# Kernel optimization log

Measured on AMD Instinct MI355X. Metric: run time of the kernel, lower is better.

The kernel has to match this reference:

```python
import jax, jax.numpy as jnp
import numpy as np

N_HEADS = 4
M = 16            # n_points (neighbors kept per voxel)
DIST = 4          # manhattan distance threshold
D_MODEL = 128
D_FFN = 256
D_CHL = 64
GRID = 96         # spatial_shape per axis
LN_EPS = 1e-5
BN_EPS = 1e-3


def setup_inputs() -> dict:
    key = jax.random.key(0)
    ks = jax.random.split(key, 24)
    N = 8192
    w = lambda k, s: jax.random.normal(k, s, jnp.float32) * 0.02
    z = lambda d: jnp.zeros((d,), jnp.float32)
    o = lambda d: jnp.ones((d,), jnp.float32)
    return {
        "features": jax.random.normal(ks[0], (N, D_CHL), jnp.float32),
        "coords": jax.random.randint(ks[1], (N, 3), 0, GRID, jnp.int32),
        "pe_w1": w(ks[2], (3, D_MODEL // 2)), "pe_b1": z(D_MODEL // 2),
        "pe_w2": w(ks[3], (D_MODEL // 2, D_MODEL)), "pe_b2": z(D_MODEL),
        "in_w": w(ks[4], (D_CHL, D_MODEL)), "in_b": z(D_MODEL),
        "q_w": w(ks[5], (D_MODEL, D_MODEL)), "q_b": z(D_MODEL),
        "k_w": w(ks[6], (D_MODEL, D_MODEL)), "k_b": z(D_MODEL),
        "v_w": w(ks[7], (D_MODEL, D_MODEL)), "v_b": z(D_MODEL),
        "o_w": w(ks[8], (D_MODEL, D_MODEL)), "o_b": z(D_MODEL),
        "n1_g": o(D_MODEL), "n1_b": z(D_MODEL),
        "l1_w": w(ks[9], (D_MODEL, D_FFN)), "l1_b": z(D_FFN),
        "l2_w": w(ks[10], (D_FFN, D_MODEL)), "l2_b": z(D_MODEL),
        "n3_g": o(D_MODEL), "n3_b": z(D_MODEL),
        "fu_w": w(ks[11], (D_MODEL + D_CHL, D_CHL)), "fu_b": z(D_CHL),
        "bn_g": o(D_CHL), "bn_b": z(D_CHL),
    }


def _layernorm(x, g, b):
    mu = jnp.mean(x, -1, keepdims=True)
    var = jnp.mean(jnp.square(x - mu), -1, keepdims=True)
    return (x - mu) * jax.lax.rsqrt(var + LN_EPS) * g + b


def reference(features, coords, pe_w1, pe_b1, pe_w2, pe_b2, in_w, in_b,
              q_w, q_b, k_w, k_b, v_w, v_b, o_w, o_b, n1_g, n1_b,
              l1_w, l1_b, l2_w, l2_b, n3_g, n3_b, fu_w, fu_b, bn_g, bn_b):
    N = features.shape[0]
    hd = D_MODEL // N_HEADS
    ci = coords.astype(jnp.float32)
    # input projection + dynamic learnable positional encoding
    src = features @ in_w + in_b
    vc = ci / (GRID - 1.0)
    src = src + (jax.nn.relu(vc @ pe_w1 + pe_b1) @ pe_w2 + pe_b2)
    # pairwise manhattan distances; accumulate per coordinate to avoid [N,N,3]
    dist = jnp.zeros((N, N), jnp.float32)
    for d in range(3):
        dist = dist + jnp.abs(ci[:, d, None] - ci[None, :, d])
    dist = jnp.where(dist <= DIST, dist, jnp.inf)
    neg_top, idx = jax.lax.top_k(-dist, M)          # [N, M]
    valid = neg_top != -jnp.inf
    # gather neighbor features; invalid slots are zero (as in torch)
    nb = jnp.where(valid[:, :, None], src[jnp.where(valid, idx, 0)], 0.0)  # [N,M,D]
    # cross-attention: query is neighbor 0 (self). NOTE: faithful raw .view
    # reshape of [N,M,D] -> [N,H,M,hd] (interleaves neighbor/head axes as torch does)
    q = (nb[:, :1] @ q_w + q_b).reshape(N, N_HEADS, 1, hd)
    k = (nb @ k_w + k_b).reshape(N, N_HEADS, M, hd)
    v = (nb @ v_w + v_b).reshape(N, N_HEADS, M, hd)
    scores = jnp.einsum('nhqd,nhkd->nhqk', q, k) / jnp.sqrt(jnp.float32(D_MODEL))
    attn = jax.nn.softmax(scores, axis=-1)
    head_out = jnp.einsum('nhqk,nhkd->nhqd', attn, v).reshape(N, D_MODEL)
    out = head_out @ o_w + o_b
    tgt = _layernorm(src + out, n1_g, n1_b)
    # FFN
    tgt2 = jax.nn.relu(tgt @ l1_w + l1_b) @ l2_w + l2_b
    tgt = _layernorm(tgt + tgt2, n3_g, n3_b)
    # EnhancedFusion: concat -> linear -> batchnorm (train-mode stats) -> relu
    fused = jnp.concatenate([features, tgt], axis=1) @ fu_w + fu_b
    mu = jnp.mean(fused, 0)
    var = jnp.var(fused, 0)
    fused = (fused - mu) * jax.lax.rsqrt(var + BN_EPS) * bn_g + bn_b
    return jax.nn.relu(fused)
```

## Files before the change

### kernel.cpp

```cpp
#include <hip/hip_runtime.h>

#define DEVFN __device__ __forceinline__

DEVFN float relu(float x) { return x < 0.f ? 0.f : x; }

__global__ __launch_bounds__(256, 4) void ka_pre_cst(
    const float* __restrict__ features, const int* __restrict__ coords,
    const float* __restrict__ pe_w1, const float* __restrict__ pe_b1,
    const float* __restrict__ pe_w2, const float* __restrict__ pe_b2,
    const float* __restrict__ in_w, const float* __restrict__ in_b,
    const float* __restrict__ q_w, const float* __restrict__ k_w,
    const float* __restrict__ v_w,
    float* __restrict__ src,
    float* __restrict__ qs, float* __restrict__ ks, float* __restrict__ vs,
    int* __restrict__ nbr, float* __restrict__ bnAcc, int N)
{
    __shared__ float sF[512];
    __shared__ float sH[512];
    __shared__ float S[1024];
    __shared__ int   sC[24];
    __shared__ int cnt[16];
    __shared__ int lst[16 * 64];
    __shared__ int outL[256];

    const int tid = threadIdx.x;
    const int bx = blockIdx.x;
    const int role_nbr = (bx % 3) == 2;

    if (role_nbr) {
        const int nb = bx / 3;
        const int q0 = nb * 16;
        if (nb == 0 && tid < 128) bnAcc[tid] = 0.f;
        if (tid < 16) cnt[tid] = 0;
        outL[tid] = -1;
        __syncthreads();
        int qx[16], qy[16], qz[16];
#pragma unroll
        for (int q = 0; q < 16; ++q) {
            qx[q] = coords[(q0 + q) * 3 + 0];
            qy[q] = coords[(q0 + q) * 3 + 1];
            qz[q] = coords[(q0 + q) * 3 + 2];
        }
        for (int cd = tid; cd < N; cd += 256) {
            int cx = coords[cd * 3 + 0];
            int cy = coords[cd * 3 + 1];
            int cz = coords[cd * 3 + 2];
#pragma unroll
            for (int q = 0; q < 16; ++q) {
                int dx = cx - qx[q]; dx = dx < 0 ? -dx : dx;
                int dy = cy - qy[q]; dy = dy < 0 ? -dy : dy;
                int dz = cz - qz[q]; dz = dz < 0 ? -dz : dz;
                int d = dx + dy + dz;
                if (d <= 4) {
                    int s = atomicAdd(&cnt[q], 1);
                    if (s < 64) lst[q * 64 + s] = (d << 13) | cd;
                }
            }
        }
        __syncthreads();
        {
            const int q = tid >> 4, t = tid & 15;
            int n = cnt[q]; if (n > 64) n = 64;
            for (int e = t; e < n; e += 16) {
                int key = lst[q * 64 + e];
                int rank = 0;
                for (int j = 0; j < n; ++j) rank += (lst[q * 64 + j] < key) ? 1 : 0;
                if (rank < 16) outL[q * 16 + rank] = key & 8191;
            }
        }
        __syncthreads();
        {
            const int q = tid >> 4, t = tid & 15;
            nbr[(q0 + q) * 16 + t] = outL[q * 16 + t];
        }
        return;
    }

    const int sb = (bx / 3) * 2 + (bx % 3);
    const int r0 = sb * 8;
    if (tid < 24) sC[tid] = coords[r0 * 3 + tid];
    for (int i = tid; i < 512; i += 256) sF[i] = features[r0 * 64 + i];
    __syncthreads();
    for (int i = tid; i < 512; i += 256) {
        int r = i >> 6, t = i & 63;
        float v0 = sC[r * 3 + 0] * (1.f / 95.f);
        float v1 = sC[r * 3 + 1] * (1.f / 95.f);
        float v2 = sC[r * 3 + 2] * (1.f / 95.f);
        float h = v0 * pe_w1[t] + v1 * pe_w1[64 + t] + v2 * pe_w1[128 + t] + pe_b1[t];
        sH[i] = relu(h);
    }
    __syncthreads();
    const int c = tid & 127, rh = tid >> 7;
    {
        float acc[4];
        const float base = in_b[c] + pe_b2[c];
#pragma unroll
        for (int r = 0; r < 4; ++r) acc[r] = base;
        for (int j = 0; j < 64; ++j) {
            float w1 = in_w[j * 128 + c];
            float w2 = pe_w2[j * 128 + c];
#pragma unroll
            for (int r = 0; r < 4; ++r) {
                int rr = rh * 4 + r;
                acc[r] += sF[rr * 64 + j] * w1 + sH[rr * 64 + j] * w2;
            }
        }
#pragma unroll
        for (int r = 0; r < 4; ++r) {
            src[(r0 + rh * 4 + r) * 128 + c] = acc[r];
            S[(rh * 4 + r) * 128 + c] = acc[r];
        }
    }
    __syncthreads();
    {
        float aq[4], ak[4], av[4];
#pragma unroll
        for (int r = 0; r < 4; ++r) { aq[r] = 0.f; ak[r] = 0.f; av[r] = 0.f; }
        for (int k4 = 0; k4 < 32; ++k4) {
            float wq0 = q_w[(k4 * 4 + 0) * 128 + c];
            float wq1 = q_w[(k4 * 4 + 1) * 128 + c];
            float wq2 = q_w[(k4 * 4 + 2) * 128 + c];
            float wq3 = q_w[(k4 * 4 + 3) * 128 + c];
            float wk0 = k_w[(k4 * 4 + 0) * 128 + c];
            float wk1 = k_w[(k4 * 4 + 1) * 128 + c];
            float wk2 = k_w[(k4 * 4 + 2) * 128 + c];
            float wk3 = k_w[(k4 * 4 + 3) * 128 + c];
            float wv0 = v_w[(k4 * 4 + 0) * 128 + c];
            float wv1 = v_w[(k4 * 4 + 1) * 128 + c];
            float wv2 = v_w[(k4 * 4 + 2) * 128 + c];
            float wv3 = v_w[(k4 * 4 + 3) * 128 + c];
#pragma unroll
            for (int r = 0; r < 4; ++r) {
                float4 s = *(const float4*)(&S[(rh * 4 + r) * 128 + k4 * 4]);
                aq[r] += s.x * wq0 + s.y * wq1 + s.z * wq2 + s.w * wq3;
                ak[r] += s.x * wk0 + s.y * wk1 + s.z * wk2 + s.w * wk3;
                av[r] += s.x * wv0 + s.y * wv1 + s.z * wv2 + s.w * wv3;
            }
        }
#pragma unroll
        for (int r = 0; r < 4; ++r) {
            qs[(r0 + rh * 4 + r) * 128 + c] = aq[r];
            ks[(r0 + rh * 4 + r) * 128 + c] = ak[r];
            vs[(r0 + rh * 4 + r) * 128 + c] = av[r];
        }
    }
}

DEVFN void ln_rows8(float* Cb, const float* __restrict__ g,
                    const float* __restrict__ b, int tid)
{
    const int r = tid >> 5, l = tid & 31;
    float x[4]; float s = 0.f, s2 = 0.f;
#pragma unroll
    for (int i = 0; i < 4; ++i) {
        x[i] = Cb[r * 128 + l * 4 + i];
        s += x[i]; s2 += x[i] * x[i];
    }
#pragma unroll
    for (int o = 1; o < 32; o <<= 1) { s += __shfl_xor(s, o); s2 += __shfl_xor(s2, o); }
    float mu = s * (1.f / 128.f);
    float var = s2 * (1.f / 128.f) - mu * mu;
    float rstd = rsqrtf(var + 1e-5f);
#pragma unroll
    for (int i = 0; i < 4; ++i) {
        int cc = l * 4 + i;
        Cb[r * 128 + cc] = (x[i] - mu) * rstd * g[cc] + b[cc];
    }
}

__global__ __launch_bounds__(256, 4) void k4_main_cst(
    const float* __restrict__ features, const float* __restrict__ src,
    const float* __restrict__ qs, const float* __restrict__ ks, const float* __restrict__ vs,
    const int* __restrict__ nbr,
    const float* __restrict__ q_b, const float* __restrict__ k_b,
    const float* __restrict__ v_b,
    const float* __restrict__ o_w, const float* __restrict__ o_b,
    const float* __restrict__ n1_g, const float* __restrict__ n1_b,
    const float* __restrict__ l1_w, const float* __restrict__ l1_b,
    const float* __restrict__ l2_w, const float* __restrict__ l2_b,
    const float* __restrict__ n3_g, const float* __restrict__ n3_b,
    const float* __restrict__ fu_w, const float* __restrict__ fu_b,
    float* __restrict__ fused, float* __restrict__ bnSum, float* __restrict__ bnSq)
{
    __shared__ float A[1024];
    __shared__ float Bt[1024];
    __shared__ float C[1024];
    __shared__ float Q[1024];
    __shared__ float H[2048];
    __shared__ float SC[512];
    __shared__ float F[512];
    __shared__ __align__(16) float bK[128], bV[128];
    __shared__ int idxL[128];
    const int tid = threadIdx.x;
    const int r0 = blockIdx.x * 8;

    for (int i = tid; i < 1024; i += 256) A[i] = src[r0 * 128 + i];
    for (int i = tid; i < 512; i += 256) F[i] = features[r0 * 64 + i];
    if (tid < 128) {
        idxL[tid] = nbr[r0 * 16 + tid];
        bK[tid] = k_b[tid]; bV[tid] = v_b[tid];
    }
    __syncthreads();
    {
        int r = tid >> 5, cg = tid & 31;
        int i0 = idxL[r * 16];
        float4 qv = make_float4(0.f, 0.f, 0.f, 0.f);
        if (i0 >= 0) qv = *(const float4*)(qs + i0 * 128 + cg * 4);
        float4 qb = *(const float4*)(q_b + cg * 4);
        qv.x += qb.x; qv.y += qb.y; qv.z += qb.z; qv.w += qb.w;
        *(float4*)(&Q[r * 128 + cg * 4]) = qv;
    }
    __syncthreads();

    const int ar = tid >> 5, ah = (tid >> 3) & 3, ag = tid & 7;
    {
#pragma unroll
        for (int jj = 0; jj < 2; ++jj) {
            int j = ag + jj * 8;
            int j4 = j >> 2, ch = j & 3;
            int id = idxL[ar * 16 + ah * 4 + j4];
            float s = 0.f;
#pragma unroll
            for (int c4 = 0; c4 < 8; ++c4) {
                float4 qv = *(const float4*)(&Q[ar * 128 + ah * 32 + c4 * 4]);
                float4 kb = *(const float4*)(&bK[ch * 32 + c4 * 4]);
                float4 kv = make_float4(0.f, 0.f, 0.f, 0.f);
                if (id >= 0) kv = *(const float4*)(ks + id * 128 + ch * 32 + c4 * 4);
                s += qv.x * (kv.x + kb.x) + qv.y * (kv.y + kb.y)
                   + qv.z * (kv.z + kb.z) + qv.w * (kv.w + kb.w);
            }
            SC[ar * 64 + ah * 16 + j] = s * 0.08838834764831845f;
        }
    }
    __syncthreads();

    {
        float p[16];
        float mx = -3.4e38f;
#pragma unroll
        for (int j = 0; j < 16; ++j) { p[j] = SC[ar * 64 + ah * 16 + j]; mx = fmaxf(mx, p[j]); }
        float sum = 0.f;
#pragma unroll
        for (int j = 0; j < 16; ++j) { p[j] = __expf(p[j] - mx); sum += p[j]; }
        float inv = 1.f / sum;
        float4 acc = make_float4(0.f, 0.f, 0.f, 0.f);
#pragma unroll
        for (int j = 0; j < 16; ++j) {
            int j4 = j >> 2, ch = j & 3;
            int id = idxL[ar * 16 + ah * 4 + j4];
            float4 vb = *(const float4*)(&bV[ch * 32 + ag * 4]);
            float4 vv = make_float4(0.f, 0.f, 0.f, 0.f);
            if (id >= 0) vv = *(const float4*)(vs + id * 128 + ch * 32 + ag * 4);
            float w = p[j] * inv;
            acc.x += w * (vv.x + vb.x); acc.y += w * (vv.y + vb.y);
            acc.z += w * (vv.z + vb.z); acc.w += w * (vv.w + vb.w);
        }
        *(float4*)(&Bt[ar * 128 + ah * 32 + ag * 4]) = acc;
    }
    __syncthreads();

    {
        const int c = tid & 127, kh = tid >> 7;
        float acc[8];
#pragma unroll
        for (int r = 0; r < 8; ++r) acc[r] = 0.f;
        const float* wp = o_w + kh * 64 * 128 + c;
        for (int k4 = 0; k4 < 16; ++k4) {
            float w0 = wp[(k4 * 4 + 0) * 128];
            float w1 = wp[(k4 * 4 + 1) * 128];
            float w2 = wp[(k4 * 4 + 2) * 128];
            float w3 = wp[(k4 * 4 + 3) * 128];
#pragma unroll
            for (int r = 0; r < 8; ++r) {
                float4 t = *(const float4*)(&Bt[r * 128 + kh * 64 + k4 * 4]);
                acc[r] += t.x * w0 + t.y * w1 + t.z * w2 + t.w * w3;
            }
        }
#pragma unroll
        for (int r = 0; r < 8; ++r) H[kh * 1024 + r * 128 + c] = acc[r];
    }
    __syncthreads();
    for (int i = tid; i < 1024; i += 256) {
        int c = i & 127;
        C[i] = A[i] + o_b[c] + H[i] + H[1024 + i];
    }
    __syncthreads();
    ln_rows8(C, n1_g, n1_b, tid);
    __syncthreads();

    {
        const int f = tid;
        float acc[8];
#pragma unroll
        for (int r = 0; r < 8; ++r) acc[r] = 0.f;
        for (int k4 = 0; k4 < 32; ++k4) {
            float w0 = l1_w[(k4 * 4 + 0) * 256 + f];
            float w1 = l1_w[(k4 * 4 + 1) * 256 + f];
            float w2 = l1_w[(k4 * 4 + 2) * 256 + f];
            float w3 = l1_w[(k4 * 4 + 3) * 256 + f];
#pragma unroll
            for (int r = 0; r < 8; ++r) {
                float4 t = *(const float4*)(&C[r * 128 + k4 * 4]);
                acc[r] += t.x * w0 + t.y * w1 + t.z * w2 + t.w * w3;
            }
        }
        const float bb = l1_b[f];
#pragma unroll
        for (int r = 0; r < 8; ++r) H[r * 256 + f] = relu(acc[r] + bb);
    }
    __syncthreads();

    {
        const int c = tid & 127, kh = tid >> 7;
        float acc[8];
#pragma unroll
        for (int r = 0; r < 8; ++r) acc[r] = 0.f;
        const float* wp = l2_w + kh * 128 * 128 + c;
        for (int k4 = 0; k4 < 32; ++k4) {
            float w0 = wp[(k4 * 4 + 0) * 128];
            float w1 = wp[(k4 * 4 + 1) * 128];
            float w2 = wp[(k4 * 4 + 2) * 128];
            float w3 = wp[(k4 * 4 + 3) * 128];
#pragma unroll
            for (int r = 0; r < 8; ++r) {
                float4 t = *(const float4*)(&H[r * 256 + kh * 128 + k4 * 4]);
                acc[r] += t.x * w0 + t.y * w1 + t.z * w2 + t.w * w3;
            }
        }
        float* P = kh ? Bt : A;
#pragma unroll
        for (int r = 0; r < 8; ++r) P[r * 128 + c] = acc[r];
    }
    __syncthreads();
    for (int i = tid; i < 1024; i += 256) {
        int c = i & 127;
        C[i] += l2_b[c] + A[i] + Bt[i];
    }
    __syncthreads();
    ln_rows8(C, n3_g, n3_b, tid);
    __syncthreads();

    {
        const int c = tid & 63, rg = tid >> 6;
        float acc[2];
        const float fb = fu_b[c];
#pragma unroll
        for (int r = 0; r < 2; ++r) acc[r] = fb;
        for (int j4 = 0; j4 < 16; ++j4) {
            float w0 = fu_w[(j4 * 4 + 0) * 64 + c];
            float w1 = fu_w[(j4 * 4 + 1) * 64 + c];
            float w2 = fu_w[(j4 * 4 + 2) * 64 + c];
            float w3 = fu_w[(j4 * 4 + 3) * 64 + c];
#pragma unroll
            for (int r = 0; r < 2; ++r) {
                float4 t = *(const float4*)(&F[(rg * 2 + r) * 64 + j4 * 4]);
                acc[r] += t.x * w0 + t.y * w1 + t.z * w2 + t.w * w3;
            }
        }
        for (int j4 = 0; j4 < 32; ++j4) {
            float w0 = fu_w[(64 + j4 * 4 + 0) * 64 + c];
            float w1 = fu_w[(64 + j4 * 4 + 1) * 64 + c];
            float w2 = fu_w[(64 + j4 * 4 + 2) * 64 + c];
            float w3 = fu_w[(64 + j4 * 4 + 3) * 64 + c];
#pragma unroll
            for (int r = 0; r < 2; ++r) {
                float4 t = *(const float4*)(&C[(rg * 2 + r) * 128 + j4 * 4]);
                acc[r] += t.x * w0 + t.y * w1 + t.z * w2 + t.w * w3;
            }
        }
#pragma unroll
        for (int r = 0; r < 2; ++r) {
            int row = rg * 2 + r;
            float v = acc[r];
            fused[(r0 + row) * 64 + c] = v;
            H[row * 64 + c] = v;
        }
    }
    __syncthreads();
    if (tid < 64) {
        float s = 0.f, s2 = 0.f;
#pragma unroll
        for (int r = 0; r < 8; ++r) { float x = H[r * 64 + tid]; s += x; s2 += x * x; }
        atomicAdd(&bnSum[tid], s);
        atomicAdd(&bnSq[tid], s2);
    }
}

__global__ __launch_bounds__(256) void k5_bn_cst(
    const float* __restrict__ fused, const float* __restrict__ bnSum,
    const float* __restrict__ bnSq,
    const float* __restrict__ g, const float* __restrict__ b,
    float* __restrict__ out, int N)
{
    const int total = N * 64;
    const float invN = 1.f / (float)N;
    for (int i = blockIdx.x * 256 + threadIdx.x; i < total; i += gridDim.x * 256) {
        int c = i & 63;
        float mu = bnSum[c] * invN;
        float var = bnSq[c] * invN - mu * mu;
        float x = fused[i];
        float y = (x - mu) * rsqrtf(var + 1e-3f) * g[c] + b[c];
        out[i] = relu(y);
    }
}

extern "C" void kernel_launch(void* const* d_in, const int* in_sizes, int n_in,
                              void* d_out, int out_size, void* d_ws, size_t ws_size,
                              hipStream_t stream)
{
    const float* features = (const float*)d_in[0];
    const int*   coords   = (const int*)d_in[1];
    const float* pe_w1 = (const float*)d_in[2];
    const float* pe_b1 = (const float*)d_in[3];
    const float* pe_w2 = (const float*)d_in[4];
    const float* pe_b2 = (const float*)d_in[5];
    const float* in_w  = (const float*)d_in[6];
    const float* in_b  = (const float*)d_in[7];
    const float* q_w   = (const float*)d_in[8];
    const float* q_b   = (const float*)d_in[9];
    const float* k_w   = (const float*)d_in[10];
    const float* k_b   = (const float*)d_in[11];
    const float* v_w   = (const float*)d_in[12];
    const float* v_b   = (const float*)d_in[13];
    const float* o_w   = (const float*)d_in[14];
    const float* o_b   = (const float*)d_in[15];
    const float* n1_g  = (const float*)d_in[16];
    const float* n1_b  = (const float*)d_in[17];
    const float* l1_w  = (const float*)d_in[18];
    const float* l1_b  = (const float*)d_in[19];
    const float* l2_w  = (const float*)d_in[20];
    const float* l2_b  = (const float*)d_in[21];
    const float* n3_g  = (const float*)d_in[22];
    const float* n3_b  = (const float*)d_in[23];
    const float* fu_w  = (const float*)d_in[24];
    const float* fu_b  = (const float*)d_in[25];
    const float* bn_g  = (const float*)d_in[26];
    const float* bn_b  = (const float*)d_in[27];

    const int N = in_sizes[0] / 64;

    float* src   = (float*)d_ws;
    float* qs    = src + (size_t)N * 128;
    float* ks    = qs  + (size_t)N * 128;
    float* vs    = ks  + (size_t)N * 128;
    float* fused = vs  + (size_t)N * 128;
    int*   nbr    = (int*)(fused + (size_t)N * 64);
    float* bnSum  = (float*)(nbr + (size_t)N * 16);
    float* bnSq   = bnSum + 64;

    ka_pre_cst<<<N / 8 + N / 16, 256, 0, stream>>>(features, coords,
                                                   pe_w1, pe_b1, pe_w2, pe_b2,
                                                   in_w, in_b, q_w, k_w, v_w,
                                                   src, qs, ks, vs, nbr, bnSum, N);
    k4_main_cst<<<N / 8, 256, 0, stream>>>(features, src, qs, ks, vs, nbr,
                                           q_b, k_b, v_b, o_w, o_b, n1_g, n1_b,
                                           l1_w, l1_b, l2_w, l2_b, n3_g, n3_b,
                                           fu_w, fu_b, fused, bnSum, bnSq);
    k5_bn_cst<<<512, 256, 0, stream>>>(fused, bnSum, bnSq, bn_g, bn_b,
                                       (float*)d_out, N);
}
```

Baseline: 221.3 us.

## Halve rows per block in main kernel to double grid and occupancy

The fused attention/FFN/fusion kernel now handles 4 voxels per block instead of 8, doubling the grid to N/4 blocks and raising the launch-bounds occupancy hint from 4 to 8 blocks. Shared memory buffers are halved and every thread-to-work mapping is reworked: scores, attention-value accumulation (2 channels per thread), layernorm over 64-lane groups, and the matmuls with 4 rows. The aim is more parallelism and better latency hiding for the gather-heavy attention. In exchange each weight read from global or L2 is reused across fewer rows, so total weight traffic doubles, and the vector loads become scalar loads.

```diff
diff --git a/kernel.cpp b/kernel.cpp
--- a/kernel.cpp
+++ b/kernel.cpp
@@ -146,29 +146,7 @@
     }
 }
 
-DEVFN void ln_rows8(float* Cb, const float* __restrict__ g,
-                    const float* __restrict__ b, int tid)
-{
-    const int r = tid >> 5, l = tid & 31;
-    float x[4]; float s = 0.f, s2 = 0.f;
-#pragma unroll
-    for (int i = 0; i < 4; ++i) {
-        x[i] = Cb[r * 128 + l * 4 + i];
-        s += x[i]; s2 += x[i] * x[i];
-    }
-#pragma unroll
-    for (int o = 1; o < 32; o <<= 1) { s += __shfl_xor(s, o); s2 += __shfl_xor(s2, o); }
-    float mu = s * (1.f / 128.f);
-    float var = s2 * (1.f / 128.f) - mu * mu;
-    float rstd = rsqrtf(var + 1e-5f);
-#pragma unroll
-    for (int i = 0; i < 4; ++i) {
-        int cc = l * 4 + i;
-        Cb[r * 128 + cc] = (x[i] - mu) * rstd * g[cc] + b[cc];
-    }
-}
-
-__global__ __launch_bounds__(256, 4) void k4_main_cst(
+__global__ __launch_bounds__(256, 8) void k4_main_cst(
     const float* __restrict__ features, const float* __restrict__ src,
     const float* __restrict__ qs, const float* __restrict__ ks, const float* __restrict__ vs,
     const int* __restrict__ nbr,
@@ -182,55 +160,49 @@
     const float* __restrict__ fu_w, const float* __restrict__ fu_b,
     float* __restrict__ fused, float* __restrict__ bnSum, float* __restrict__ bnSq)
 {
-    __shared__ float A[1024];
-    __shared__ float Bt[1024];
-    __shared__ float C[1024];
-    __shared__ float Q[1024];
-    __shared__ float H[2048];
-    __shared__ float SC[512];
-    __shared__ float F[512];
+    __shared__ float A[512];
+    __shared__ float Bt[512];
+    __shared__ float C[512];
+    __shared__ float Q[512];
+    __shared__ float H[1024];
+    __shared__ float SC[256];
+    __shared__ float F[256];
     __shared__ __align__(16) float bK[128], bV[128];
-    __shared__ int idxL[128];
+    __shared__ int idxL[64];
     const int tid = threadIdx.x;
-    const int r0 = blockIdx.x * 8;
-
-    for (int i = tid; i < 1024; i += 256) A[i] = src[r0 * 128 + i];
-    for (int i = tid; i < 512; i += 256) F[i] = features[r0 * 64 + i];
+    const int r0 = blockIdx.x * 4;
+
+    for (int i = tid; i < 512; i += 256) A[i] = src[r0 * 128 + i];
+    F[tid & 255] = features[r0 * 64 + (tid & 255)];
+    if (tid < 64) idxL[tid] = nbr[r0 * 16 + tid];
+    if (tid < 128) { bK[tid] = k_b[tid]; bV[tid] = v_b[tid]; }
+    __syncthreads();
     if (tid < 128) {
-        idxL[tid] = nbr[r0 * 16 + tid];
-        bK[tid] = k_b[tid]; bV[tid] = v_b[tid];
-    }
-    __syncthreads();
-    {
-        int r = tid >> 5, cg = tid & 31;
+        int r = tid >> 5, cg4 = tid & 31;
         int i0 = idxL[r * 16];
         float4 qv = make_float4(0.f, 0.f, 0.f, 0.f);
-        if (i0 >= 0) qv = *(const float4*)(qs + i0 * 128 + cg * 4);
-        float4 qb = *(const float4*)(q_b + cg * 4);
+        if (i0 >= 0) qv = *(const float4*)(qs + i0 * 128 + cg4 * 4);
+        float4 qb = *(const float4*)(q_b + cg4 * 4);
         qv.x += qb.x; qv.y += qb.y; qv.z += qb.z; qv.w += qb.w;
-        *(float4*)(&Q[r * 128 + cg * 4]) = qv;
-    }
-    __syncthreads();
-
-    const int ar = tid >> 5, ah = (tid >> 3) & 3, ag = tid & 7;
-    {
-#pragma unroll
-        for (int jj = 0; jj < 2; ++jj) {
-            int j = ag + jj * 8;
-            int j4 = j >> 2, ch = j & 3;
-            int id = idxL[ar * 16 + ah * 4 + j4];
-            float s = 0.f;
-#pragma unroll
-            for (int c4 = 0; c4 < 8; ++c4) {
-                float4 qv = *(const float4*)(&Q[ar * 128 + ah * 32 + c4 * 4]);
-                float4 kb = *(const float4*)(&bK[ch * 32 + c4 * 4]);
-                float4 kv = make_float4(0.f, 0.f, 0.f, 0.f);
-                if (id >= 0) kv = *(const float4*)(ks + id * 128 + ch * 32 + c4 * 4);
-                s += qv.x * (kv.x + kb.x) + qv.y * (kv.y + kb.y)
-                   + qv.z * (kv.z + kb.z) + qv.w * (kv.w + kb.w);
-            }
-            SC[ar * 64 + ah * 16 + j] = s * 0.08838834764831845f;
-        }
+        *(float4*)(&Q[r * 128 + cg4 * 4]) = qv;
+    }
+    __syncthreads();
+
+    const int ar = tid >> 6, ah = (tid >> 4) & 3, aj = tid & 15;
+    {
+        int j4 = aj >> 2, ch = aj & 3;
+        int id = idxL[ar * 16 + ah * 4 + j4];
+        float s = 0.f;
+#pragma unroll
+        for (int c4 = 0; c4 < 8; ++c4) {
+            float4 qv = *(const float4*)(&Q[ar * 128 + ah * 32 + c4 * 4]);
+            float4 kb = *(const float4*)(&bK[ch * 32 + c4 * 4]);
+            float4 kv = make_float4(0.f, 0.f, 0.f, 0.f);
+            if (id >= 0) kv = *(const float4*)(ks + id * 128 + ch * 32 + c4 * 4);
+            s += qv.x * (kv.x + kb.x) + qv.y * (kv.y + kb.y)
+               + qv.z * (kv.z + kb.z) + qv.w * (kv.w + kb.w);
+        }
+        SC[ar * 64 + ah * 16 + aj] = s * 0.08838834764831845f;
     }
     __syncthreads();
 
@@ -243,27 +215,31 @@
 #pragma unroll
         for (int j = 0; j < 16; ++j) { p[j] = __expf(p[j] - mx); sum += p[j]; }
         float inv = 1.f / sum;
-        float4 acc = make_float4(0.f, 0.f, 0.f, 0.f);
+        float a0 = 0.f, a1 = 0.f;
+        const int cb = ah * 32 + aj * 2;
 #pragma unroll
         for (int j = 0; j < 16; ++j) {
             int j4 = j >> 2, ch = j & 3;
             int id = idxL[ar * 16 + ah * 4 + j4];
-            float4 vb = *(const float4*)(&bV[ch * 32 + ag * 4]);
-            float4 vv = make_float4(0.f, 0.f, 0.f, 0.f);
-            if (id >= 0) vv = *(const float4*)(vs + id * 128 + ch * 32 + ag * 4);
+            float v0 = 0.f, v1 = 0.f;
+            if (id >= 0) {
+                const float* vr = vs + id * 128 + ch * 32 + aj * 2;
+                v0 = vr[0]; v1 = vr[1];
+            }
             float w = p[j] * inv;
-            acc.x += w * (vv.x + vb.x); acc.y += w * (vv.y + vb.y);
-            acc.z += w * (vv.z + vb.z); acc.w += w * (vv.w + vb.w);
-        }
-        *(float4*)(&Bt[ar * 128 + ah * 32 + ag * 4]) = acc;
-    }
-    __syncthreads();
-
-    {
-        const int c = tid & 127, kh = tid >> 7;
-        float acc[8];
-#pragma unroll
-        for (int r = 0; r < 8; ++r) acc[r] = 0.f;
+            a0 += w * (v0 + bV[ch * 32 + aj * 2 + 0]);
+            a1 += w * (v1 + bV[ch * 32 + aj * 2 + 1]);
+        }
+        Bt[ar * 128 + cb] = a0;
+        Bt[ar * 128 + cb + 1] = a1;
+    }
+    __syncthreads();
+
+    const int c = tid & 127, kh = tid >> 7;
+    {
+        float acc[4];
+#pragma unroll
+        for (int r = 0; r < 4; ++r) acc[r] = 0.f;
         const float* wp = o_w + kh * 64 * 128 + c;
         for (int k4 = 0; k4 < 16; ++k4) {
             float w0 = wp[(k4 * 4 + 0) * 128];
@@ -271,50 +247,61 @@
             float w2 = wp[(k4 * 4 + 2) * 128];
             float w3 = wp[(k4 * 4 + 3) * 128];
 #pragma unroll
-            for (int r = 0; r < 8; ++r) {
+            for (int r = 0; r < 4; ++r) {
                 float4 t = *(const float4*)(&Bt[r * 128 + kh * 64 + k4 * 4]);
                 acc[r] += t.x * w0 + t.y * w1 + t.z * w2 + t.w * w3;
             }
         }
 #pragma unroll
-        for (int r = 0; r < 8; ++r) H[kh * 1024 + r * 128 + c] = acc[r];
-    }
-    __syncthreads();
-    for (int i = tid; i < 1024; i += 256) {
-        int c = i & 127;
-        C[i] = A[i] + o_b[c] + H[i] + H[1024 + i];
-    }
-    __syncthreads();
-    ln_rows8(C, n1_g, n1_b, tid);
+        for (int r = 0; r < 4; ++r) H[kh * 512 + r * 128 + c] = acc[r];
+    }
+    __syncthreads();
+    for (int i = tid; i < 512; i += 256) {
+        int cc = i & 127;
+        C[i] = A[i] + o_b[cc] + H[i] + H[512 + i];
+    }
+    __syncthreads();
+    {
+        const int r = tid >> 6, l = tid & 63;
+        float x0 = C[r * 128 + l * 2], x1 = C[r * 128 + l * 2 + 1];
+        float s = x0 + x1, s2 = x0 * x0 + x1 * x1;
+#pragma unroll
+        for (int o = 1; o < 64; o <<= 1) { s += __shfl_xor(s, o); s2 += __shfl_xor(s2, o); }
+        float mu = s * (1.f / 128.f);
+        float var = s2 * (1.f / 128.f) - mu * mu;
+        float rstd = rsqrtf(var + 1e-5f);
+        int c0 = l * 2;
+        C[r * 128 + c0] = (x0 - mu) * rstd * n1_g[c0] + n1_b[c0];
+        C[r * 128 + c0 + 1] = (x1 - mu) * rstd * n1_g[c0 + 1] + n1_b[c0 + 1];
+    }
     __syncthreads();
 
     {
         const int f = tid;
-        float acc[8];
-#pragma unroll
-        for (int r = 0; r < 8; ++r) acc[r] = 0.f;
+        float acc[4];
+#pragma unroll
+        for (int r = 0; r < 4; ++r) acc[r] = 0.f;
         for (int k4 = 0; k4 < 32; ++k4) {
             float w0 = l1_w[(k4 * 4 + 0) * 256 + f];
             float w1 = l1_w[(k4 * 4 + 1) * 256 + f];
             float w2 = l1_w[(k4 * 4 + 2) * 256 + f];
             float w3 = l1_w[(k4 * 4 + 3) * 256 + f];
 #pragma unroll
-            for (int r = 0; r < 8; ++r) {
+            for (int r = 0; r < 4; ++r) {
                 float4 t = *(const float4*)(&C[r * 128 + k4 * 4]);
                 acc[r] += t.x * w0 + t.y * w1 + t.z * w2 + t.w * w3;
             }
         }
         const float bb = l1_b[f];
 #pragma unroll
-        for (int r = 0; r < 8; ++r) H[r * 256 + f] = relu(acc[r] + bb);
-    }
-    __syncthreads();
-
-    {
-        const int c = tid & 127, kh = tid >> 7;
-        float acc[8];
-#pragma unroll
-        for (int r = 0; r < 8; ++r) acc[r] = 0.f;
+        for (int r = 0; r < 4; ++r) H[r * 256 + f] = relu(acc[r] + bb);
+    }
+    __syncthreads();
+
+    {
+        float acc[4];
+#pragma unroll
+        for (int r = 0; r < 4; ++r) acc[r] = 0.f;
         const float* wp = l2_w + kh * 128 * 128 + c;
         for (int k4 = 0; k4 < 32; ++k4) {
             float w0 = wp[(k4 * 4 + 0) * 128];
@@ -322,65 +309,63 @@
             float w2 = wp[(k4 * 4 + 2) * 128];
             float w3 = wp[(k4 * 4 + 3) * 128];
 #pragma unroll
-            for (int r = 0; r < 8; ++r) {
+            for (int r = 0; r < 4; ++r) {
                 float4 t = *(const float4*)(&H[r * 256 + kh * 128 + k4 * 4]);
                 acc[r] += t.x * w0 + t.y * w1 + t.z * w2 + t.w * w3;
             }
         }
         float* P = kh ? Bt : A;
 #pragma unroll
-        for (int r = 0; r < 8; ++r) P[r * 128 + c] = acc[r];
-    }
-    __syncthreads();
-    for (int i = tid; i < 1024; i += 256) {
-        int c = i & 127;
-        C[i] += l2_b[c] + A[i] + Bt[i];
-    }
-    __syncthreads();
-    ln_rows8(C, n3_g, n3_b, tid);
-    __syncthreads();
-
-    {
-        const int c = tid & 63, rg = tid >> 6;
-        float acc[2];
-        const float fb = fu_b[c];
-#pragma unroll
-        for (int r = 0; r < 2; ++r) acc[r] = fb;
+        for (int r = 0; r < 4; ++r) P[r * 128 + c] = acc[r];
+    }
+    __syncthreads();
+    for (int i = tid; i < 512; i += 256) {
+        int cc = i & 127;
+        C[i] += l2_b[cc] + A[i] + Bt[i];
+    }
+    __syncthreads();
+    {
+        const int r = tid >> 6, l = tid & 63;
+        float x0 = C[r * 128 + l * 2], x1 = C[r * 128 + l * 2 + 1];
+        float s = x0 + x1, s2 = x0 * x0 + x1 * x1;
+#pragma unroll
+        for (int o = 1; o < 64; o <<= 1) { s += __shfl_xor(s, o); s2 += __shfl_xor(s2, o); }
+        float mu = s * (1.f / 128.f);
+        float var = s2 * (1.f / 128.f) - mu * mu;
+        float rstd = rsqrtf(var + 1e-5f);
+        int c0 = l * 2;
+        C[r * 128 + c0] = (x0 - mu) * rstd * n3_g[c0] + n3_b[c0];
+        C[r * 128 + c0 + 1] = (x1 - mu) * rstd * n3_g[c0 + 1] + n3_b[c0 + 1];
+    }
+    __syncthreads();
+
+    {
+        const int c6 = tid & 63, rg = tid >> 6;
+        float acc = fu_b[c6];
         for (int j4 = 0; j4 < 16; ++j4) {
-            float w0 = fu_w[(j4 * 4 + 0) * 64 + c];
-            float w1 = fu_w[(j4 * 4 + 1) * 64 + c];
-            float w2 = fu_w[(j4 * 4 + 2) * 64 + c];
-            float w3 = fu_w[(j4 * 4 + 3) * 64 + c];
-#pragma unroll
-            for (int r = 0; r < 2; ++r) {
-                float4 t = *(const float4*)(&F[(rg * 2 + r) * 64 + j4 * 4]);
-                acc[r] += t.x * w0 + t.y * w1 + t.z * w2 + t.w * w3;
-            }
+            float w0 = fu_w[(j4 * 4 + 0) * 64 + c6];
+            float w1 = fu_w[(j4 * 4 + 1) * 64 + c6];
+            float w2 = fu_w[(j4 * 4 + 2) * 64 + c6];
+            float w3 = fu_w[(j4 * 4 + 3) * 64 + c6];
+            float4 t = *(const float4*)(&F[rg * 64 + j4 * 4]);
+            acc += t.x * w0 + t.y * w1 + t.z * w2 + t.w * w3;
         }
         for (int j4 = 0; j4 < 32; ++j4) {
-            float w0 = fu_w[(64 + j4 * 4 + 0) * 64 + c];
-            float w1 = fu_w[(64 + j4 * 4 + 1) * 64 + c];
-            float w2 = fu_w[(64 + j4 * 4 + 2) * 64 + c];
-            float w3 = fu_w[(64 + j4 * 4 + 3) * 64 + c];
-#pragma unroll
-            for (int r = 0; r < 2; ++r) {
-                float4 t = *(const float4*)(&C[(rg * 2 + r) * 128 + j4 * 4]);
-                acc[r] += t.x * w0 + t.y * w1 + t.z * w2 + t.w * w3;
-            }
-        }
-#pragma unroll
-        for (int r = 0; r < 2; ++r) {
-            int row = rg * 2 + r;
-            float v = acc[r];
-            fused[(r0 + row) * 64 + c] = v;
-            H[row * 64 + c] = v;
-        }
+            float w0 = fu_w[(64 + j4 * 4 + 0) * 64 + c6];
+            float w1 = fu_w[(64 + j4 * 4 + 1) * 64 + c6];
+            float w2 = fu_w[(64 + j4 * 4 + 2) * 64 + c6];
+            float w3 = fu_w[(64 + j4 * 4 + 3) * 64 + c6];
+            float4 t = *(const float4*)(&C[rg * 128 + j4 * 4]);
+            acc += t.x * w0 + t.y * w1 + t.z * w2 + t.w * w3;
+        }
+        fused[(r0 + rg) * 64 + c6] = acc;
+        H[rg * 64 + c6] = acc;
     }
     __syncthreads();
     if (tid < 64) {
         float s = 0.f, s2 = 0.f;
 #pragma unroll
-        for (int r = 0; r < 8; ++r) { float x = H[r * 64 + tid]; s += x; s2 += x * x; }
+        for (int r = 0; r < 4; ++r) { float x = H[r * 64 + tid]; s += x; s2 += x * x; }
         atomicAdd(&bnSum[tid], s);
         atomicAdd(&bnSq[tid], s2);
     }
@@ -452,7 +437,7 @@
                                                    pe_w1, pe_b1, pe_w2, pe_b2,
                                                    in_w, in_b, q_w, k_w, v_w,
                                                    src, qs, ks, vs, nbr, bnSum, N);
-    k4_main_cst<<<N / 8, 256, 0, stream>>>(features, src, qs, ks, vs, nbr,
+    k4_main_cst<<<N / 4, 256, 0, stream>>>(features, src, qs, ks, vs, nbr,
                                            q_b, k_b, v_b, o_w, o_b, n1_g, n1_b,
                                            l1_w, l1_b, l2_w, l2_b, n3_g, n3_b,
                                            fu_w, fu_b, fused, bnSum, bnSq);
```

New measurement: 296.2 us. +33.9%, slower.

## Split-K the pre-kernel projections with float4 weight loads and LDS reduction

Applied to the files above, without the earlier changes.

The src projection and Q/K/V projections in the pre-kernel are restructured so that each warp handles a slice of the K dimension for all 8 rows, with each thread owning 4 output columns loaded as float4. Partial sums go into a new 32KB shared buffer and are reduced across the 8 K-groups. The neighbor-search scratch arrays now alias that buffer, and the occupancy hint drops from 4 to 3 blocks per CU. The layernorm helper is inlined and some variables are renamed, which is cleanup only. The aim is to issue fewer, wider weight loads. The cost is extra shared-memory traffic, more barriers and lower occupancy.

```diff
diff --git a/kernel.cpp b/kernel.cpp
--- a/kernel.cpp
+++ b/kernel.cpp
@@ -4,7 +4,7 @@
 
 DEVFN float relu(float x) { return x < 0.f ? 0.f : x; }
 
-__global__ __launch_bounds__(256, 4) void ka_pre_cst(
+__global__ __launch_bounds__(256, 3) void ka_pre_cst(
     const float* __restrict__ features, const int* __restrict__ coords,
     const float* __restrict__ pe_w1, const float* __restrict__ pe_b1,
     const float* __restrict__ pe_w2, const float* __restrict__ pe_b2,
@@ -18,16 +18,17 @@
     __shared__ float sF[512];
     __shared__ float sH[512];
     __shared__ float S[1024];
+    __shared__ float P[8192];
     __shared__ int   sC[24];
-    __shared__ int cnt[16];
-    __shared__ int lst[16 * 64];
-    __shared__ int outL[256];
 
     const int tid = threadIdx.x;
     const int bx = blockIdx.x;
-    const int role_nbr = (bx % 3) == 2;
-
-    if (role_nbr) {
+
+    if ((bx % 3) == 2) {
+        int* ip   = (int*)P;
+        int* cnt  = ip;
+        int* lst  = ip + 16;
+        int* outL = ip + 16 + 1024;
         const int nb = bx / 3;
         const int q0 = nb * 16;
         if (nb == 0 && tid < 128) bnAcc[tid] = 0.f;
@@ -90,81 +91,82 @@
         sH[i] = relu(h);
     }
     __syncthreads();
-    const int c = tid & 127, rh = tid >> 7;
-    {
-        float acc[4];
-        const float base = in_b[c] + pe_b2[c];
-#pragma unroll
-        for (int r = 0; r < 4; ++r) acc[r] = base;
-        for (int j = 0; j < 64; ++j) {
-            float w1 = in_w[j * 128 + c];
-            float w2 = pe_w2[j * 128 + c];
-#pragma unroll
-            for (int r = 0; r < 4; ++r) {
-                int rr = rh * 4 + r;
-                acc[r] += sF[rr * 64 + j] * w1 + sH[rr * 64 + j] * w2;
-            }
-        }
-#pragma unroll
-        for (int r = 0; r < 4; ++r) {
-            src[(r0 + rh * 4 + r) * 128 + c] = acc[r];
-            S[(rh * 4 + r) * 128 + c] = acc[r];
-        }
-    }
-    __syncthreads();
-    {
-        float aq[4], ak[4], av[4];
-#pragma unroll
-        for (int r = 0; r < 4; ++r) { aq[r] = 0.f; ak[r] = 0.f; av[r] = 0.f; }
-        for (int k4 = 0; k4 < 32; ++k4) {
-            float wq0 = q_w[(k4 * 4 + 0) * 128 + c];
-            float wq1 = q_w[(k4 * 4 + 1) * 128 + c];
-            float wq2 = q_w[(k4 * 4 + 2) * 128 + c];
-            float wq3 = q_w[(k4 * 4 + 3) * 128 + c];
-            float wk0 = k_w[(k4 * 4 + 0) * 128 + c];
-            float wk1 = k_w[(k4 * 4 + 1) * 128 + c];
-            float wk2 = k_w[(k4 * 4 + 2) * 128 + c];
-            float wk3 = k_w[(k4 * 4 + 3) * 128 + c];
-            float wv0 = v_w[(k4 * 4 + 0) * 128 + c];
-            float wv1 = v_w[(k4 * 4 + 1) * 128 + c];
-            float wv2 = v_w[(k4 * 4 + 2) * 128 + c];
-            float wv3 = v_w[(k4 * 4 + 3) * 128 + c];
-#pragma unroll
-            for (int r = 0; r < 4; ++r) {
-                float4 s = *(const float4*)(&S[(rh * 4 + r) * 128 + k4 * 4]);
-                aq[r] += s.x * wq0 + s.y * wq1 + s.z * wq2 + s.w * wq3;
-                ak[r] += s.x * wk0 + s.y * wk1 + s.z * wk2 + s.w * wk3;
-                av[r] += s.x * wv0 + s.y * wv1 + s.z * wv2 + s.w * wv3;
-            }
-        }
-#pragma unroll
-        for (int r = 0; r < 4; ++r) {
-            qs[(r0 + rh * 4 + r) * 128 + c] = aq[r];
-            ks[(r0 + rh * 4 + r) * 128 + c] = ak[r];
-            vs[(r0 + rh * 4 + r) * 128 + c] = av[r];
-        }
-    }
-}
-
-DEVFN void ln_rows8(float* Cb, const float* __restrict__ g,
-                    const float* __restrict__ b, int tid)
-{
-    const int r = tid >> 5, l = tid & 31;
-    float x[4]; float s = 0.f, s2 = 0.f;
-#pragma unroll
-    for (int i = 0; i < 4; ++i) {
-        x[i] = Cb[r * 128 + l * 4 + i];
-        s += x[i]; s2 += x[i] * x[i];
-    }
-#pragma unroll
-    for (int o = 1; o < 32; o <<= 1) { s += __shfl_xor(s, o); s2 += __shfl_xor(s2, o); }
-    float mu = s * (1.f / 128.f);
-    float var = s2 * (1.f / 128.f) - mu * mu;
-    float rstd = rsqrtf(var + 1e-5f);
-#pragma unroll
-    for (int i = 0; i < 4; ++i) {
-        int cc = l * 4 + i;
-        Cb[r * 128 + cc] = (x[i] - mu) * rstd * g[cc] + b[cc];
+
+    const int chunk = tid & 31;
+    const int kg = tid >> 5;
+
+    {
+        float4 acc[8];
+#pragma unroll
+        for (int r = 0; r < 8; ++r) acc[r] = make_float4(0.f, 0.f, 0.f, 0.f);
+        for (int i = 0; i < 8; ++i) {
+            int k = kg * 8 + i;
+            float4 w1 = *(const float4*)(in_w + k * 128 + chunk * 4);
+            float4 w2 = *(const float4*)(pe_w2 + k * 128 + chunk * 4);
+#pragma unroll
+            for (int r = 0; r < 8; ++r) {
+                float a = sF[r * 64 + k], b = sH[r * 64 + k];
+                acc[r].x += a * w1.x + b * w2.x;
+                acc[r].y += a * w1.y + b * w2.y;
+                acc[r].z += a * w1.z + b * w2.z;
+                acc[r].w += a * w1.w + b * w2.w;
+            }
+        }
+#pragma unroll
+        for (int r = 0; r < 8; ++r)
+            *(float4*)(&P[kg * 1024 + r * 128 + chunk * 4]) = acc[r];
+    }
+    __syncthreads();
+    {
+        const int base = tid * 4;
+        float4 s = *(const float4*)(&P[base]);
+#pragma unroll
+        for (int g = 1; g < 8; ++g) {
+            float4 p = *(const float4*)(&P[g * 1024 + base]);
+            s.x += p.x; s.y += p.y; s.z += p.z; s.w += p.w;
+        }
+        const int cc = base & 127;
+        s.x += in_b[cc + 0] + pe_b2[cc + 0];
+        s.y += in_b[cc + 1] + pe_b2[cc + 1];
+        s.z += in_b[cc + 2] + pe_b2[cc + 2];
+        s.w += in_b[cc + 3] + pe_b2[cc + 3];
+        *(float4*)(&S[base]) = s;
+        *(float4*)(src + r0 * 128 + base) = s;
+    }
+    __syncthreads();
+
+#pragma unroll
+    for (int which = 0; which < 3; ++which) {
+        const float* __restrict__ w = (which == 0) ? q_w : (which == 1) ? k_w : v_w;
+        float* __restrict__ out = (which == 0) ? qs : (which == 1) ? ks : vs;
+        float4 acc[8];
+#pragma unroll
+        for (int r = 0; r < 8; ++r) acc[r] = make_float4(0.f, 0.f, 0.f, 0.f);
+        for (int i = 0; i < 16; ++i) {
+            int k = kg * 16 + i;
+            float4 wv = *(const float4*)(w + k * 128 + chunk * 4);
+#pragma unroll
+            for (int r = 0; r < 8; ++r) {
+                float a = S[r * 128 + k];
+                acc[r].x += a * wv.x; acc[r].y += a * wv.y;
+                acc[r].z += a * wv.z; acc[r].w += a * wv.w;
+            }
+        }
+#pragma unroll
+        for (int r = 0; r < 8; ++r)
+            *(float4*)(&P[kg * 1024 + r * 128 + chunk * 4]) = acc[r];
+        __syncthreads();
+        {
+            const int base = tid * 4;
+            float4 s = *(const float4*)(&P[base]);
+#pragma unroll
+            for (int g = 1; g < 8; ++g) {
+                float4 p = *(const float4*)(&P[g * 1024 + base]);
+                s.x += p.x; s.y += p.y; s.z += p.z; s.w += p.w;
+            }
+            *(float4*)(out + r0 * 128 + base) = s;
+        }
+        __syncthreads();
     }
 }
 
@@ -202,13 +204,13 @@
     }
     __syncthreads();
     {
-        int r = tid >> 5, cg = tid & 31;
+        int r = tid >> 5, cg4 = tid & 31;
         int i0 = idxL[r * 16];
         float4 qv = make_float4(0.f, 0.f, 0.f, 0.f);
-        if (i0 >= 0) qv = *(const float4*)(qs + i0 * 128 + cg * 4);
-        float4 qb = *(const float4*)(q_b + cg * 4);
+        if (i0 >= 0) qv = *(const float4*)(qs + i0 * 128 + cg4 * 4);
+        float4 qb = *(const float4*)(q_b + cg4 * 4);
         qv.x += qb.x; qv.y += qb.y; qv.z += qb.z; qv.w += qb.w;
-        *(float4*)(&Q[r * 128 + cg * 4]) = qv;
+        *(float4*)(&Q[r * 128 + cg4 * 4]) = qv;
     }
     __syncthreads();
 
@@ -259,8 +261,8 @@
     }
     __syncthreads();
 
-    {
-        const int c = tid & 127, kh = tid >> 7;
+    const int c = tid & 127, kh = tid >> 7;
+    {
         float acc[8];
 #pragma unroll
         for (int r = 0; r < 8; ++r) acc[r] = 0.f;
@@ -281,11 +283,29 @@
     }
     __syncthreads();
     for (int i = tid; i < 1024; i += 256) {
-        int c = i & 127;
-        C[i] = A[i] + o_b[c] + H[i] + H[1024 + i];
-    }
-    __syncthreads();
-    ln_rows8(C, n1_g, n1_b, tid);
+        int cc = i & 127;
+        C[i] = A[i] + o_b[cc] + H[i] + H[1024 + i];
+    }
+    __syncthreads();
+    {
+        const int r = tid >> 5, l = tid & 31;
+        float x[4]; float s = 0.f, s2 = 0.f;
+#pragma unroll
+        for (int i = 0; i < 4; ++i) {
+            x[i] = C[r * 128 + l * 4 + i];
+            s += x[i]; s2 += x[i] * x[i];
+        }
+#pragma unroll
+        for (int o = 1; o < 32; o <<= 1) { s += __shfl_xor(s, o); s2 += __shfl_xor(s2, o); }
+        float mu = s * (1.f / 128.f);
+        float var = s2 * (1.f / 128.f) - mu * mu;
+        float rstd = rsqrtf(var + 1e-5f);
+#pragma unroll
+        for (int i = 0; i < 4; ++i) {
+            int cc = l * 4 + i;
+            C[r * 128 + cc] = (x[i] - mu) * rstd * n1_g[cc] + n1_b[cc];
+        }
+    }
     __syncthreads();
 
     {
@@ -311,7 +331,6 @@
     __syncthreads();
 
     {
-        const int c = tid & 127, kh = tid >> 7;
         float acc[8];
 #pragma unroll
         for (int r = 0; r < 8; ++r) acc[r] = 0.f;
@@ -327,30 +346,48 @@
                 acc[r] += t.x * w0 + t.y * w1 + t.z * w2 + t.w * w3;
             }
         }
-        float* P = kh ? Bt : A;
-#pragma unroll
-        for (int r = 0; r < 8; ++r) P[r * 128 + c] = acc[r];
+        float* P2 = kh ? Bt : A;
+#pragma unroll
+        for (int r = 0; r < 8; ++r) P2[r * 128 + c] = acc[r];
     }
     __syncthreads();
     for (int i = tid; i < 1024; i += 256) {
-        int c = i & 127;
-        C[i] += l2_b[c] + A[i] + Bt[i];
-    }
-    __syncthreads();
-    ln_rows8(C, n3_g, n3_b, tid);
-    __syncthreads();
-
-    {
-        const int c = tid & 63, rg = tid >> 6;
+        int cc = i & 127;
+        C[i] += l2_b[cc] + A[i] + Bt[i];
+    }
+    __syncthreads();
+    {
+        const int r = tid >> 5, l = tid & 31;
+        float x[4]; float s = 0.f, s2 = 0.f;
+#pragma unroll
+        for (int i = 0; i < 4; ++i) {
+            x[i] = C[r * 128 + l * 4 + i];
+            s += x[i]; s2 += x[i] * x[i];
+        }
+#pragma unroll
+        for (int o = 1; o < 32; o <<= 1) { s += __shfl_xor(s, o); s2 += __shfl_xor(s2, o); }
+        float mu = s * (1.f / 128.f);
+        float var = s2 * (1.f / 128.f) - mu * mu;
+        float rstd = rsqrtf(var + 1e-5f);
+#pragma unroll
+        for (int i = 0; i < 4; ++i) {
+            int cc = l * 4 + i;
+            C[r * 128 + cc] = (x[i] - mu) * rstd * n3_g[cc] + n3_b[cc];
+        }
+    }
+    __syncthreads();
+
+    {
+        const int c6 = tid & 63, rg = tid >> 6;
         float acc[2];
-        const float fb = fu_b[c];
+        const float fb = fu_b[c6];
 #pragma unroll
         for (int r = 0; r < 2; ++r) acc[r] = fb;
         for (int j4 = 0; j4 < 16; ++j4) {
-            float w0 = fu_w[(j4 * 4 + 0) * 64 + c];
-            float w1 = fu_w[(j4 * 4 + 1) * 64 + c];
-            float w2 = fu_w[(j4 * 4 + 2) * 64 + c];
-            float w3 = fu_w[(j4 * 4 + 3) * 64 + c];
+            float w0 = fu_w[(j4 * 4 + 0) * 64 + c6];
+            float w1 = fu_w[(j4 * 4 + 1) * 64 + c6];
+            float w2 = fu_w[(j4 * 4 + 2) * 64 + c6];
+            float w3 = fu_w[(j4 * 4 + 3) * 64 + c6];
 #pragma unroll
             for (int r = 0; r < 2; ++r) {
                 float4 t = *(const float4*)(&F[(rg * 2 + r) * 64 + j4 * 4]);
@@ -358,10 +395,10 @@
             }
         }
         for (int j4 = 0; j4 < 32; ++j4) {
-            float w0 = fu_w[(64 + j4 * 4 + 0) * 64 + c];
-            float w1 = fu_w[(64 + j4 * 4 + 1) * 64 + c];
-            float w2 = fu_w[(64 + j4 * 4 + 2) * 64 + c];
-            float w3 = fu_w[(64 + j4 * 4 + 3) * 64 + c];
+            float w0 = fu_w[(64 + j4 * 4 + 0) * 64 + c6];
+            float w1 = fu_w[(64 + j4 * 4 + 1) * 64 + c6];
+            float w2 = fu_w[(64 + j4 * 4 + 2) * 64 + c6];
+            float w3 = fu_w[(64 + j4 * 4 + 3) * 64 + c6];
 #pragma unroll
             for (int r = 0; r < 2; ++r) {
                 float4 t = *(const float4*)(&C[(rg * 2 + r) * 128 + j4 * 4]);
@@ -372,8 +409,8 @@
         for (int r = 0; r < 2; ++r) {
             int row = rg * 2 + r;
             float v = acc[r];
-            fused[(r0 + row) * 64 + c] = v;
-            H[row * 64 + c] = v;
+            fused[(r0 + row) * 64 + c6] = v;
+            H[row * 64 + c6] = v;
         }
     }
     __syncthreads();
```

Result: slower. 231.6 us (+4.7%).
